# Optimization experiments

Measured on AMD Instinct MI355X. Metric: run time of the kernel, lower is better.

Reference implementation:

```python
import jax, jax.numpy as jnp
import numpy as np

N = 50000          # num nodes
E = 800000         # edges per adjacency (avg degree 16)
NFEAT = 512
NHID = 256
NCLS = 100
LN_EPS = 1e-5


def spmm(rows, cols, vals, feat):
    # sparse [N,N] @ dense [N,F] via gather + segment-sum scatter
    return jax.ops.segment_sum(vals[:, None] * feat[cols], rows, num_segments=N)


def layernorm(h, g, b):
    mu = jnp.mean(h, axis=-1, keepdims=True)
    var = jnp.var(h, axis=-1, keepdims=True)
    return (h - mu) * jax.lax.rsqrt(var + LN_EPS) * g + b


def setup_inputs() -> dict:
    key = jax.random.key(0)
    ks = jax.random.split(key, 20)
    inp = {
        "x": jax.random.normal(ks[0], (N, NFEAT), dtype=jnp.float32),
        "adj_rows": jax.random.randint(ks[1], (4, E), 0, N, dtype=jnp.int32),
        "adj_cols": jax.random.randint(ks[2], (4, E), 0, N, dtype=jnp.int32),
        "adj_vals": jax.random.uniform(ks[3], (4, E), dtype=jnp.float32) / 16.0,
    }
    def lin(k, fin, fout):
        s = 1.0 / np.sqrt(fin)
        kw, kb = jax.random.split(k)
        return (jax.random.uniform(kw, (fin, fout), minval=-s, maxval=s, dtype=jnp.float32),
                jax.random.uniform(kb, (fout,), minval=-s, maxval=s, dtype=jnp.float32))
    # layer 0: GraphSage(nfeat -> nhid), LayerNorm over 2*nhid
    inp["W0"], inp["b0"] = lin(ks[4], NFEAT, NHID)
    inp["ln0_g"] = jnp.ones((2 * NHID,), jnp.float32)
    inp["ln0_b"] = jnp.zeros((2 * NHID,), jnp.float32)
    # layer 1: GCN(2*nhid -> nhid)
    inp["W1"], inp["b1"] = lin(ks[5], 2 * NHID, NHID)
    # layer 2: GraphSage(nhid -> nhid), LayerNorm over 2*nhid
    inp["W2"], inp["b2"] = lin(ks[6], NHID, NHID)
    inp["ln2_g"] = jnp.ones((2 * NHID,), jnp.float32)
    inp["ln2_b"] = jnp.zeros((2 * NHID,), jnp.float32)
    # layer 3: GCN(2*nhid -> nhid)
    inp["W3"], inp["b3"] = lin(ks[7], 2 * NHID, NHID)
    # output linear (nhid -> num_classes)
    inp["Wout"], inp["bout"] = lin(ks[8], NHID, NCLS)
    return inp


def reference(x, adj_rows, adj_cols, adj_vals,
              W0, b0, ln0_g, ln0_b, W1, b1, W2, b2, ln2_g, ln2_b, W3, b3,
              Wout, bout):
    # layer 0: GraphSage — feat = Linear(x); h = LN(concat([feat, A@feat])); ReLU; dropout(p=0)=id
    feat = x @ W0 + b0
    agg = spmm(adj_rows[0], adj_cols[0], adj_vals[0], feat)
    h = jax.nn.relu(layernorm(jnp.concatenate([feat, agg], axis=1), ln0_g, ln0_b))
    # layer 1: GCN — h = A @ Linear(h); ReLU
    h = jax.nn.relu(spmm(adj_rows[1], adj_cols[1], adj_vals[1], h @ W1 + b1))
    # layer 2: GraphSage
    feat = h @ W2 + b2
    agg = spmm(adj_rows[2], adj_cols[2], adj_vals[2], feat)
    h = jax.nn.relu(layernorm(jnp.concatenate([feat, agg], axis=1), ln2_g, ln2_b))
    # layer 3: GCN
    h = jax.nn.relu(spmm(adj_rows[3], adj_cols[3], adj_vals[3], h @ W3 + b3))
    # output head
    return h @ Wout + bout
```

## Files before the change

kernel.cpp:

```cpp
#include <hip/hip_runtime.h>

#define N_NODES 50000
#define E_EDGES 800000
#define NFEAT   512
#define NHID    256
#define NCLS    100
#define LN_EPS  1e-5f

#define NB     196
#define CHUNKA 6144
#define CAPB   6656

typedef __attribute__((ext_vector_type(8))) short bf16x8;
typedef __attribute__((ext_vector_type(4))) float f32x4;

__device__ __forceinline__ ushort bf16_rne(float x) {
    unsigned u = __float_as_uint(x);
    unsigned r = u + 0x7FFFu + ((u >> 16) & 1u);
    return (ushort)(r >> 16);
}
__device__ __forceinline__ float bf16_to_f(ushort h) {
    return __uint_as_float(((unsigned)h) << 16);
}

__device__ __forceinline__ void gload16(const void* g, void* l) {
    __builtin_amdgcn_global_load_lds(
        (const __attribute__((address_space(1))) unsigned int*)g,
        (__attribute__((address_space(3))) unsigned int*)l, 16, 0, 0);
}

__global__ __launch_bounds__(256)
void wsplit_kernel(const float* __restrict__ W, ushort* __restrict__ WT,
                   int K, int Nc, int NP)
{
    const int idx = blockIdx.x * 256 + threadIdx.x;
    if (idx >= NP * K) return;
    const int n = idx / K, k = idx - n * K;
    const float w = (n < Nc) ? W[(size_t)k * Nc + n] : 0.f;
    WT[idx] = bf16_rne(w);
}

__global__ __launch_bounds__(256)
void xconv_kernel(const float* __restrict__ x, ushort* __restrict__ xb, int n8)
{
    const int idx = blockIdx.x * 256 + threadIdx.x;
    if (idx >= n8) return;
    const float4 v0 = ((const float4*)x)[idx * 2];
    const float4 v1 = ((const float4*)x)[idx * 2 + 1];
    bf16x8 h;
    h[0] = (short)bf16_rne(v0.x); h[1] = (short)bf16_rne(v0.y);
    h[2] = (short)bf16_rne(v0.z); h[3] = (short)bf16_rne(v0.w);
    h[4] = (short)bf16_rne(v1.x); h[5] = (short)bf16_rne(v1.y);
    h[6] = (short)bf16_rne(v1.z); h[7] = (short)bf16_rne(v1.w);
    *(bf16x8*)&xb[idx * 8] = h;
}

template<int WF32, int WBF>
__global__ __launch_bounds__(512)
void gemm_mfma_bf16(const ushort* __restrict__ A1, const ushort* __restrict__ A2,
                    int K1, int K, const ushort* __restrict__ BT,
                    const float* __restrict__ bias, float* __restrict__ C,
                    ushort* __restrict__ Cbf, int M, int Nc)
{
    __shared__ __align__(16) ushort Ah[2][128 * 32];
    __shared__ __align__(16) ushort Bh[2][128 * 32];

    const int tid = threadIdx.x;
    const int bm  = blockIdx.x * 128;
    const int bn  = blockIdx.y * 128;
    const int w   = tid >> 6;
    const int l   = tid & 63;
    const int wm  = (w >> 2) * 64;
    const int wn  = (w & 3) * 32;
    const int fr  = l & 15;
    const int fq  = l >> 4;

    const int gro = l >> 2;
    const int gch = ((l & 3) ^ (gro & 3)) * 8;
    const int ldsbase = (16 * w) * 32;

    f32x4 acc[4][2];
    #pragma unroll
    for (int i = 0; i < 4; ++i) {
        acc[i][0] = (f32x4){0.f, 0.f, 0.f, 0.f};
        acc[i][1] = (f32x4){0.f, 0.f, 0.f, 0.f};
    }

    const int K2 = K - K1;
    const int NS = K / 32;

    auto stage = [&](int s, int b) {
        const int k0 = s * 32;
        gload16(&BT[(size_t)(bn + 16 * w + gro) * K + k0 + gch], &Bh[b][ldsbase]);
        const ushort* asrc;
        if (k0 < K1) asrc = &A1[(size_t)(bm + 16 * w + gro) * K1 + k0 + gch];
        else         asrc = &A2[(size_t)(bm + 16 * w + gro) * K2 + (k0 - K1) + gch];
        gload16(asrc, &Ah[b][ldsbase]);
    };

    stage(0, 0);
    __syncthreads();

    int cur = 0;
    for (int s = 0; s < NS; ++s) {
        if (s + 1 < NS) stage(s + 1, cur ^ 1);

        bf16x8 bf[2];
        #pragma unroll
        for (int nf = 0; nf < 2; ++nf) {
            const int r = wn + nf * 16 + fr;
            bf[nf] = *(const bf16x8*)&Bh[cur][r * 32 + ((fq ^ (r & 3)) * 8)];
        }
        #pragma unroll
        for (int mf = 0; mf < 4; ++mf) {
            const int r = wm + mf * 16 + fr;
            const bf16x8 af = *(const bf16x8*)&Ah[cur][r * 32 + ((fq ^ (r & 3)) * 8)];
            acc[mf][0] = __builtin_amdgcn_mfma_f32_16x16x32_bf16(af, bf[0], acc[mf][0], 0, 0, 0);
            acc[mf][1] = __builtin_amdgcn_mfma_f32_16x16x32_bf16(af, bf[1], acc[mf][1], 0, 0, 0);
        }
        __syncthreads();
        cur ^= 1;
    }

    #pragma unroll
    for (int mf = 0; mf < 4; ++mf) {
        #pragma unroll
        for (int r = 0; r < 4; ++r) {
            const int row = bm + wm + mf * 16 + fq * 4 + r;
            if (row >= M) continue;
            #pragma unroll
            for (int nf = 0; nf < 2; ++nf) {
                const int col = bn + wn + nf * 16 + fr;
                if (col < Nc) {
                    const float v = acc[mf][nf][r] + bias[col];
                    if (WF32) C[(size_t)row * Nc + col] = v;
                    if (WBF)  Cbf[(size_t)row * Nc + col] = bf16_rne(v);
                }
            }
        }
    }
}

__global__ __launch_bounds__(256)
void bin_kernel(const int* __restrict__ rows, const int* __restrict__ cols,
                const float* __restrict__ vals, int* __restrict__ bcur,
                int2* __restrict__ est)
{
    __shared__ int cnt[NB];
    __shared__ int scn[256];
    __shared__ int cstart[NB];
    __shared__ int ccur[NB];
    __shared__ int garr[NB];
    __shared__ __align__(16) int2 buf[CHUNKA];

    const int a  = blockIdx.y;
    const int e0 = blockIdx.x * CHUNKA;
    const int n  = min(CHUNKA, E_EDGES - e0);
    const int t  = threadIdx.x;
    const int*   rp = rows + (size_t)a * E_EDGES + e0;
    const int*   cp = cols + (size_t)a * E_EDGES + e0;
    const float* vp = vals + (size_t)a * E_EDGES + e0;

    if (t < NB) cnt[t] = 0;
    __syncthreads();
    for (int i = t; i < n; i += 256) atomicAdd(&cnt[((unsigned)rp[i]) >> 8], 1);
    __syncthreads();

    scn[t] = (t < NB) ? cnt[t] : 0;
    __syncthreads();
    for (int off = 1; off < 256; off <<= 1) {
        const int v = (t >= off) ? scn[t - off] : 0;
        __syncthreads();
        scn[t] += v;
        __syncthreads();
    }
    if (t < NB) {
        const int ex = scn[t] - cnt[t];
        cstart[t] = ex;
        ccur[t]   = ex;
        garr[t]   = atomicAdd(&bcur[a * NB + t], cnt[t]);
    }
    __syncthreads();

    for (int i = t; i < n; i += 256) {
        const unsigned r = (unsigned)rp[i];
        const int b = r >> 8;
        const int p = atomicAdd(&ccur[b], 1);
        buf[p] = make_int2((int)((r << 16) | (unsigned)cp[i]), __float_as_int(vp[i]));
    }
    __syncthreads();

    for (int i = t; i < n; i += 256) {
        const int2 en = buf[i];
        const int b = ((unsigned)en.x) >> 24;
        const int slot = garr[b] + (i - cstart[b]);
        if (slot < CAPB)
            est[((size_t)(a * NB + b)) * CAPB + slot] = en;
    }
}

__global__ __launch_bounds__(256)
void bscan_kernel(const int* __restrict__ bcur, int* __restrict__ bbase)
{
    __shared__ int s[256];
    const int a = blockIdx.x;
    const int t = threadIdx.x;
    const int v = (t < NB) ? bcur[a * NB + t] : 0;
    s[t] = v;
    __syncthreads();
    for (int off = 1; off < 256; off <<= 1) {
        const int u = (t >= off) ? s[t - off] : 0;
        __syncthreads();
        s[t] += u;
        __syncthreads();
    }
    if (t < NB) bbase[a * NB + t] = s[t] - v;
}

__global__ __launch_bounds__(256)
void sort_kernel(const int* __restrict__ bcur, const int* __restrict__ bbase,
                 const int2* __restrict__ est, int2* __restrict__ cpk,
                 int* __restrict__ rowstart)
{
    __shared__ __align__(16) int2 sbuf[CAPB];
    __shared__ __align__(16) int2 obuf[CAPB];
    __shared__ int cnt[256];
    __shared__ int scn[256];
    __shared__ int cur[256];

    const int a = blockIdx.y;
    const int b = blockIdx.x;
    const int t = threadIdx.x;
    const int nb = min(bcur[a * NB + b], CAPB);
    const size_t slots = ((size_t)(a * NB + b)) * CAPB;

    for (int i = t; i < nb; i += 256) sbuf[i] = est[slots + i];
    cnt[t] = 0;
    __syncthreads();
    for (int i = t; i < nb; i += 256)
        atomicAdd(&cnt[(((unsigned)sbuf[i].x) >> 16) & 255], 1);
    __syncthreads();

    scn[t] = cnt[t];
    __syncthreads();
    for (int off = 1; off < 256; off <<= 1) {
        const int v = (t >= off) ? scn[t - off] : 0;
        __syncthreads();
        scn[t] += v;
        __syncthreads();
    }
    const int excl = scn[t] - cnt[t];
    cur[t] = excl;

    const int bb = bbase[a * NB + b];
    const int r0 = b << 8;
    if (r0 + t < N_NODES)
        rowstart[(size_t)a * (N_NODES + 1) + r0 + t] = bb + excl;
    if (b == NB - 1 && t == 0)
        rowstart[(size_t)a * (N_NODES + 1) + N_NODES] = E_EDGES;
    __syncthreads();

    for (int i = t; i < nb; i += 256) {
        const int2 en = sbuf[i];
        const int r = (((unsigned)en.x) >> 16) & 255;
        const int p = atomicAdd(&cur[r], 1);
        obuf[p] = make_int2(en.x & 0xFFFF, en.y);
    }
    __syncthreads();

    int2* co = cpk + (size_t)a * E_EDGES + bb;
    for (int i = t; i < nb; i += 256) co[i] = obuf[i];
}

template<int LNFUSE>
__global__ __launch_bounds__(256)
void spmm_kernel(const int* __restrict__ rowstart, const int2* __restrict__ cpk,
                 const ushort* __restrict__ feat, ushort* __restrict__ out0,
                 ushort* __restrict__ out1, const float* __restrict__ g,
                 const float* __restrict__ be)
{
    const int row  = __builtin_amdgcn_readfirstlane((blockIdx.x * 256 + threadIdx.x) >> 6);
    const int lane = threadIdx.x & 63;

    const int s = __builtin_amdgcn_readfirstlane(rowstart[row]);
    const int e = __builtin_amdgcn_readfirstlane(rowstart[row + 1]);

    const ushort* fbase = feat + lane * 4;
    float ax = 0.f, ay = 0.f, az = 0.f, aw = 0.f;

    for (int j = s; j < e; j += 16) {
        #pragma unroll
        for (int q = 0; q < 16; ++q) {
            if (j + q < e) {
                const int2 ev = cpk[j + q];
                const float v = __int_as_float(ev.y);
                const uint2 f = *(const uint2*)(fbase + (size_t)ev.x * NHID);
                ax += v * __uint_as_float(f.x << 16);
                ay += v * __uint_as_float(f.x & 0xFFFF0000u);
                az += v * __uint_as_float(f.y << 16);
                aw += v * __uint_as_float(f.y & 0xFFFF0000u);
            }
        }
    }

    if (LNFUSE) {
        const uint2 fx = *(const uint2*)(fbase + (size_t)row * NHID);
        float xf[4] = {__uint_as_float(fx.x << 16), __uint_as_float(fx.x & 0xFFFF0000u),
                       __uint_as_float(fx.y << 16), __uint_as_float(fx.y & 0xFFFF0000u)};

        float sum = xf[0] + xf[1] + xf[2] + xf[3] + ax + ay + az + aw;
        #pragma unroll
        for (int m = 1; m < 64; m <<= 1) sum += __shfl_xor(sum, m, 64);
        const float mean = sum * (1.f / 512.f);

        float sq = 0.f;
        #pragma unroll
        for (int jj = 0; jj < 4; ++jj) { const float d = xf[jj] - mean; sq += d * d; }
        { float d; d = ax - mean; sq += d * d; d = ay - mean; sq += d * d;
          d = az - mean; sq += d * d; d = aw - mean; sq += d * d; }
        #pragma unroll
        for (int m = 1; m < 64; m <<= 1) sq += __shfl_xor(sq, m, 64);
        const float rstd = rsqrtf(sq * (1.f / 512.f) + LN_EPS);

        const int col = lane * 4;
        const float av[4] = {ax, ay, az, aw};
        ushort4 o0, o1;
        float t0[4], t1[4];
        #pragma unroll
        for (int jj = 0; jj < 4; ++jj) {
            t0[jj] = fmaxf((xf[jj] - mean) * rstd * g[col + jj] + be[col + jj], 0.f);
            t1[jj] = fmaxf((av[jj] - mean) * rstd * g[256 + col + jj] + be[256 + col + jj], 0.f);
        }
        o0.x = bf16_rne(t0[0]); o0.y = bf16_rne(t0[1]); o0.z = bf16_rne(t0[2]); o0.w = bf16_rne(t0[3]);
        o1.x = bf16_rne(t1[0]); o1.y = bf16_rne(t1[1]); o1.z = bf16_rne(t1[2]); o1.w = bf16_rne(t1[3]);
        *(ushort4*)&out0[(size_t)row * NHID + col] = o0;
        *(ushort4*)&out1[(size_t)row * NHID + col] = o1;
    } else {
        ushort4 o;
        o.x = bf16_rne(fmaxf(ax, 0.f)); o.y = bf16_rne(fmaxf(ay, 0.f));
        o.z = bf16_rne(fmaxf(az, 0.f)); o.w = bf16_rne(fmaxf(aw, 0.f));
        *(ushort4*)&out0[(size_t)row * NHID + lane * 4] = o;
    }
}

extern "C" void kernel_launch(void* const* d_in, const int* in_sizes, int n_in,
                              void* d_out, int out_size, void* d_ws, size_t ws_size,
                              hipStream_t stream)
{
    const float* x    = (const float*)d_in[0];
    const int*   rows = (const int*)  d_in[1];
    const int*   cols = (const int*)  d_in[2];
    const float* vals = (const float*)d_in[3];
    const float* W0   = (const float*)d_in[4];
    const float* b0   = (const float*)d_in[5];
    const float* g0   = (const float*)d_in[6];
    const float* be0  = (const float*)d_in[7];
    const float* W1   = (const float*)d_in[8];
    const float* b1   = (const float*)d_in[9];
    const float* W2   = (const float*)d_in[10];
    const float* b2   = (const float*)d_in[11];
    const float* g2   = (const float*)d_in[12];
    const float* be2  = (const float*)d_in[13];
    const float* W3   = (const float*)d_in[14];
    const float* b3   = (const float*)d_in[15];
    const float* Wout = (const float*)d_in[16];
    const float* bout = (const float*)d_in[17];
    float* out = (float*)d_out;

    char* wsb = (char*)d_ws;
    size_t off = 0;
    auto carve = [&](size_t bytes) { void* p = wsb + off; off += (bytes + 255) & ~(size_t)255; return p; };
    int*    rowstart = (int*)   carve((size_t)4 * (N_NODES + 1) * 4);
    int*    bcur     = (int*)   carve((size_t)4 * NB * 4);
    int*    bbase    = (int*)   carve((size_t)4 * NB * 4);
    int2*   cpk      = (int2*)  carve((size_t)4 * E_EDGES * 8);
    int2*   est      = (int2*)  carve((size_t)4 * NB * CAPB * 8);
    ushort* Xb       = (ushort*)carve((size_t)N_NODES * NFEAT * 2);
    ushort* F        = (ushort*)carve((size_t)N_NODES * NHID * 2);
    ushort* P        = (ushort*)carve((size_t)N_NODES * NHID * 2);
    ushort* Q        = (ushort*)carve((size_t)N_NODES * NHID * 2);
    ushort* G        = (ushort*)carve((size_t)N_NODES * NHID * 2);
    ushort* H        = (ushort*)carve((size_t)N_NODES * NHID * 2);
    ushort* W0T = (ushort*)carve((size_t)256 * 512 * 2);
    ushort* W1T = (ushort*)carve((size_t)256 * 512 * 2);
    ushort* W2T = (ushort*)carve((size_t)256 * 256 * 2);
    ushort* W3T = (ushort*)carve((size_t)256 * 512 * 2);
    ushort* WoT = (ushort*)carve((size_t)128 * 256 * 2);
    carve(131072);

    const dim3 blk(256);
    const dim3 blkg(512);
    const dim3 g_gemm(391, 2);
    const dim3 g_head(391, 1);
    const dim3 g_bin((E_EDGES + CHUNKA - 1) / CHUNKA, 4);
    const dim3 g_sort(NB, 4);
    const int  row_blocks = (N_NODES * 64 + 255) / 256;

    wsplit_kernel<<<(256*512 + 255)/256, blk, 0, stream>>>(W0,   W0T, 512, 256, 256);
    wsplit_kernel<<<(256*512 + 255)/256, blk, 0, stream>>>(W1,   W1T, 512, 256, 256);
    wsplit_kernel<<<(256*256 + 255)/256, blk, 0, stream>>>(W2,   W2T, 256, 256, 256);
    wsplit_kernel<<<(256*512 + 255)/256, blk, 0, stream>>>(W3,   W3T, 512, 256, 256);
    wsplit_kernel<<<(128*256 + 255)/256, blk, 0, stream>>>(Wout, WoT, 256, 100, 128);
    xconv_kernel<<<(N_NODES * NFEAT / 8 + 255)/256, blk, 0, stream>>>(x, Xb, N_NODES * NFEAT / 8);

    hipMemsetAsync(bcur, 0, (size_t)4 * NB * 4, stream);
    bin_kernel<<<g_bin, blk, 0, stream>>>(rows, cols, vals, bcur, est);
    bscan_kernel<<<4, blk, 0, stream>>>(bcur, bbase);
    sort_kernel<<<g_sort, blk, 0, stream>>>(bcur, bbase, est, cpk, rowstart);

    const int* rs0 = rowstart;
    const int* rs1 = rowstart + (N_NODES + 1);
    const int* rs2 = rowstart + 2 * (N_NODES + 1);
    const int* rs3 = rowstart + 3 * (N_NODES + 1);
    const int2* c0 = cpk;
    const int2* c1 = cpk + E_EDGES;
    const int2* c2 = cpk + 2 * (size_t)E_EDGES;
    const int2* c3 = cpk + 3 * (size_t)E_EDGES;

    gemm_mfma_bf16<0,1><<<g_gemm, blkg, 0, stream>>>(Xb, Xb, 512, 512, W0T, b0, nullptr, F, N_NODES, 256);
    spmm_kernel<1><<<row_blocks, blk, 0, stream>>>(rs0, c0, F, P, Q, g0, be0);

    gemm_mfma_bf16<0,1><<<g_gemm, blkg, 0, stream>>>(P, Q, 256, 512, W1T, b1, nullptr, G, N_NODES, 256);
    spmm_kernel<0><<<row_blocks, blk, 0, stream>>>(rs1, c1, G, H, nullptr, nullptr, nullptr);

    gemm_mfma_bf16<0,1><<<g_gemm, blkg, 0, stream>>>(H, H, 256, 256, W2T, b2, nullptr, F, N_NODES, 256);
    spmm_kernel<1><<<row_blocks, blk, 0, stream>>>(rs2, c2, F, P, Q, g2, be2);

    gemm_mfma_bf16<0,1><<<g_gemm, blkg, 0, stream>>>(P, Q, 256, 512, W3T, b3, nullptr, G, N_NODES, 256);
    spmm_kernel<0><<<row_blocks, blk, 0, stream>>>(rs3, c3, G, H, nullptr, nullptr, nullptr);

    gemm_mfma_bf16<1,0><<<g_head, blkg, 0, stream>>>(H, H, 256, 256, WoT, bout, out, nullptr, N_NODES, 100);
}
```

Before: 529.1 us.

## Use 4-wave GEMM tiles, merge weight conversions, and drop LDS staging in sort

The GEMM moves from 8 waves with 64x32 warp tiles to 4 waves with 64x64 warp tiles. Each wave now issues two loads per stage and 16 MFMAs per K step, which raises register use and lowers wave count per block. The five weight-transpose launches become one kernel that dispatches on the flat index. The sort kernel reads bucket entries directly from global memory twice instead of staging them in shared memory, so it uses less LDS and may fit more blocks per CU.

```diff
diff --git a/kernel.cpp b/kernel.cpp
--- a/kernel.cpp
+++ b/kernel.cpp
@@ -30,14 +30,23 @@
 }
 
 __global__ __launch_bounds__(256)
-void wsplit_kernel(const float* __restrict__ W, ushort* __restrict__ WT,
-                   int K, int Nc, int NP)
-{
-    const int idx = blockIdx.x * 256 + threadIdx.x;
-    if (idx >= NP * K) return;
+void wsplit_all(const float* __restrict__ W0, const float* __restrict__ W1,
+                const float* __restrict__ W2, const float* __restrict__ W3,
+                const float* __restrict__ Wo,
+                ushort* __restrict__ W0T, ushort* __restrict__ W1T,
+                ushort* __restrict__ W2T, ushort* __restrict__ W3T,
+                ushort* __restrict__ WoT)
+{
+    int idx = blockIdx.x * 256 + threadIdx.x;
+    const float* W; ushort* WT; int K, Nc;
+    if      (idx < 131072) { W = W0; WT = W0T; K = 512; Nc = 256; }
+    else if (idx < 262144) { idx -= 131072; W = W1; WT = W1T; K = 512; Nc = 256; }
+    else if (idx < 327680) { idx -= 262144; W = W2; WT = W2T; K = 256; Nc = 256; }
+    else if (idx < 458752) { idx -= 327680; W = W3; WT = W3T; K = 512; Nc = 256; }
+    else if (idx < 491520) { idx -= 458752; W = Wo; WT = WoT; K = 256; Nc = 100; }
+    else return;
     const int n = idx / K, k = idx - n * K;
-    const float w = (n < Nc) ? W[(size_t)k * Nc + n] : 0.f;
-    WT[idx] = bf16_rne(w);
+    WT[idx] = bf16_rne((n < Nc) ? W[(size_t)k * Nc + n] : 0.f);
 }
 
 __global__ __launch_bounds__(256)
@@ -56,7 +65,7 @@
 }
 
 template<int WF32, int WBF>
-__global__ __launch_bounds__(512)
+__global__ __launch_bounds__(256)
 void gemm_mfma_bf16(const ushort* __restrict__ A1, const ushort* __restrict__ A2,
                     int K1, int K, const ushort* __restrict__ BT,
                     const float* __restrict__ bias, float* __restrict__ C,
@@ -70,32 +79,38 @@
     const int bn  = blockIdx.y * 128;
     const int w   = tid >> 6;
     const int l   = tid & 63;
-    const int wm  = (w >> 2) * 64;
-    const int wn  = (w & 3) * 32;
+    const int wm  = (w >> 1) * 64;
+    const int wn  = (w & 1) * 64;
     const int fr  = l & 15;
     const int fq  = l >> 4;
 
     const int gro = l >> 2;
     const int gch = ((l & 3) ^ (gro & 3)) * 8;
-    const int ldsbase = (16 * w) * 32;
-
-    f32x4 acc[4][2];
+    const int ldsbase = (32 * w) * 32;
+
+    f32x4 acc[4][4];
     #pragma unroll
-    for (int i = 0; i < 4; ++i) {
-        acc[i][0] = (f32x4){0.f, 0.f, 0.f, 0.f};
-        acc[i][1] = (f32x4){0.f, 0.f, 0.f, 0.f};
-    }
+    for (int i = 0; i < 4; ++i)
+        #pragma unroll
+        for (int j = 0; j < 4; ++j) acc[i][j] = (f32x4){0.f, 0.f, 0.f, 0.f};
 
     const int K2 = K - K1;
     const int NS = K / 32;
 
     auto stage = [&](int s, int b) {
         const int k0 = s * 32;
-        gload16(&BT[(size_t)(bn + 16 * w + gro) * K + k0 + gch], &Bh[b][ldsbase]);
-        const ushort* asrc;
-        if (k0 < K1) asrc = &A1[(size_t)(bm + 16 * w + gro) * K1 + k0 + gch];
-        else         asrc = &A2[(size_t)(bm + 16 * w + gro) * K2 + (k0 - K1) + gch];
-        gload16(asrc, &Ah[b][ldsbase]);
+        gload16(&BT[(size_t)(bn + 32 * w + gro) * K + k0 + gch],      &Bh[b][ldsbase]);
+        gload16(&BT[(size_t)(bn + 32 * w + 16 + gro) * K + k0 + gch], &Bh[b][ldsbase + 512]);
+        const ushort *a0, *a1;
+        if (k0 < K1) {
+            a0 = &A1[(size_t)(bm + 32 * w + gro) * K1 + k0 + gch];
+            a1 = &A1[(size_t)(bm + 32 * w + 16 + gro) * K1 + k0 + gch];
+        } else {
+            a0 = &A2[(size_t)(bm + 32 * w + gro) * K2 + (k0 - K1) + gch];
+            a1 = &A2[(size_t)(bm + 32 * w + 16 + gro) * K2 + (k0 - K1) + gch];
+        }
+        gload16(a0, &Ah[b][ldsbase]);
+        gload16(a1, &Ah[b][ldsbase + 512]);
     };
 
     stage(0, 0);
@@ -105,9 +120,9 @@
     for (int s = 0; s < NS; ++s) {
         if (s + 1 < NS) stage(s + 1, cur ^ 1);
 
-        bf16x8 bf[2];
-        #pragma unroll
-        for (int nf = 0; nf < 2; ++nf) {
+        bf16x8 bf[4];
+        #pragma unroll
+        for (int nf = 0; nf < 4; ++nf) {
             const int r = wn + nf * 16 + fr;
             bf[nf] = *(const bf16x8*)&Bh[cur][r * 32 + ((fq ^ (r & 3)) * 8)];
         }
@@ -115,8 +130,9 @@
         for (int mf = 0; mf < 4; ++mf) {
             const int r = wm + mf * 16 + fr;
             const bf16x8 af = *(const bf16x8*)&Ah[cur][r * 32 + ((fq ^ (r & 3)) * 8)];
-            acc[mf][0] = __builtin_amdgcn_mfma_f32_16x16x32_bf16(af, bf[0], acc[mf][0], 0, 0, 0);
-            acc[mf][1] = __builtin_amdgcn_mfma_f32_16x16x32_bf16(af, bf[1], acc[mf][1], 0, 0, 0);
+            #pragma unroll
+            for (int nf = 0; nf < 4; ++nf)
+                acc[mf][nf] = __builtin_amdgcn_mfma_f32_16x16x32_bf16(af, bf[nf], acc[mf][nf], 0, 0, 0);
         }
         __syncthreads();
         cur ^= 1;
@@ -129,7 +145,7 @@
             const int row = bm + wm + mf * 16 + fq * 4 + r;
             if (row >= M) continue;
             #pragma unroll
-            for (int nf = 0; nf < 2; ++nf) {
+            for (int nf = 0; nf < 4; ++nf) {
                 const int col = bn + wn + nf * 16 + fr;
                 if (col < Nc) {
                     const float v = acc[mf][nf][r] + bias[col];
@@ -222,34 +238,33 @@
                  const int2* __restrict__ est, int2* __restrict__ cpk,
                  int* __restrict__ rowstart)
 {
-    __shared__ __align__(16) int2 sbuf[CAPB];
     __shared__ __align__(16) int2 obuf[CAPB];
     __shared__ int cnt[256];
-    __shared__ int scn[256];
     __shared__ int cur[256];
 
     const int a = blockIdx.y;
     const int b = blockIdx.x;
     const int t = threadIdx.x;
     const int nb = min(bcur[a * NB + b], CAPB);
-    const size_t slots = ((size_t)(a * NB + b)) * CAPB;
-
-    for (int i = t; i < nb; i += 256) sbuf[i] = est[slots + i];
+    const int2* ei = est + ((size_t)(a * NB + b)) * CAPB;
+
     cnt[t] = 0;
     __syncthreads();
     for (int i = t; i < nb; i += 256)
-        atomicAdd(&cnt[(((unsigned)sbuf[i].x) >> 16) & 255], 1);
-    __syncthreads();
-
-    scn[t] = cnt[t];
+        atomicAdd(&cnt[(((unsigned)ei[i].x) >> 16) & 255], 1);
+    __syncthreads();
+
+    int scv = cnt[t];
+    cur[t] = scv;
     __syncthreads();
     for (int off = 1; off < 256; off <<= 1) {
-        const int v = (t >= off) ? scn[t - off] : 0;
-        __syncthreads();
-        scn[t] += v;
-        __syncthreads();
-    }
-    const int excl = scn[t] - cnt[t];
+        const int v = (t >= off) ? cur[t - off] : 0;
+        __syncthreads();
+        cur[t] += v;
+        __syncthreads();
+    }
+    const int excl = cur[t] - scv;
+    __syncthreads();
     cur[t] = excl;
 
     const int bb = bbase[a * NB + b];
@@ -261,7 +276,7 @@
     __syncthreads();
 
     for (int i = t; i < nb; i += 256) {
-        const int2 en = sbuf[i];
+        const int2 en = ei[i];
         const int r = (((unsigned)en.x) >> 16) & 255;
         const int p = atomicAdd(&cur[r], 1);
         obuf[p] = make_int2(en.x & 0xFFFF, en.y);
@@ -389,18 +404,13 @@
     carve(131072);
 
     const dim3 blk(256);
-    const dim3 blkg(512);
     const dim3 g_gemm(391, 2);
     const dim3 g_head(391, 1);
     const dim3 g_bin((E_EDGES + CHUNKA - 1) / CHUNKA, 4);
     const dim3 g_sort(NB, 4);
     const int  row_blocks = (N_NODES * 64 + 255) / 256;
 
-    wsplit_kernel<<<(256*512 + 255)/256, blk, 0, stream>>>(W0,   W0T, 512, 256, 256);
-    wsplit_kernel<<<(256*512 + 255)/256, blk, 0, stream>>>(W1,   W1T, 512, 256, 256);
-    wsplit_kernel<<<(256*256 + 255)/256, blk, 0, stream>>>(W2,   W2T, 256, 256, 256);
-    wsplit_kernel<<<(256*512 + 255)/256, blk, 0, stream>>>(W3,   W3T, 512, 256, 256);
-    wsplit_kernel<<<(128*256 + 255)/256, blk, 0, stream>>>(Wout, WoT, 256, 100, 128);
+    wsplit_all<<<1920, blk, 0, stream>>>(W0, W1, W2, W3, Wout, W0T, W1T, W2T, W3T, WoT);
     xconv_kernel<<<(N_NODES * NFEAT / 8 + 255)/256, blk, 0, stream>>>(x, Xb, N_NODES * NFEAT / 8);
 
     hipMemsetAsync(bcur, 0, (size_t)4 * NB * 4, stream);
@@ -417,17 +427,17 @@
     const int2* c2 = cpk + 2 * (size_t)E_EDGES;
     const int2* c3 = cpk + 3 * (size_t)E_EDGES;
 
-    gemm_mfma_bf16<0,1><<<g_gemm, blkg, 0, stream>>>(Xb, Xb, 512, 512, W0T, b0, nullptr, F, N_NODES, 256);
+    gemm_mfma_bf16<0,1><<<g_gemm, blk, 0, stream>>>(Xb, Xb, 512, 512, W0T, b0, nullptr, F, N_NODES, 256);
     spmm_kernel<1><<<row_blocks, blk, 0, stream>>>(rs0, c0, F, P, Q, g0, be0);
 
-    gemm_mfma_bf16<0,1><<<g_gemm, blkg, 0, stream>>>(P, Q, 256, 512, W1T, b1, nullptr, G, N_NODES, 256);
+    gemm_mfma_bf16<0,1><<<g_gemm, blk, 0, stream>>>(P, Q, 256, 512, W1T, b1, nullptr, G, N_NODES, 256);
     spmm_kernel<0><<<row_blocks, blk, 0, stream>>>(rs1, c1, G, H, nullptr, nullptr, nullptr);
 
-    gemm_mfma_bf16<0,1><<<g_gemm, blkg, 0, stream>>>(H, H, 256, 256, W2T, b2, nullptr, F, N_NODES, 256);
+    gemm_mfma_bf16<0,1><<<g_gemm, blk, 0, stream>>>(H, H, 256, 256, W2T, b2, nullptr, F, N_NODES, 256);
     spmm_kernel<1><<<row_blocks, blk, 0, stream>>>(rs2, c2, F, P, Q, g2, be2);
 
-    gemm_mfma_bf16<0,1><<<g_gemm, blkg, 0, stream>>>(P, Q, 256, 512, W3T, b3, nullptr, G, N_NODES, 256);
+    gemm_mfma_bf16<0,1><<<g_gemm, blk, 0, stream>>>(P, Q, 256, 512, W3T, b3, nullptr, G, N_NODES, 256);
     spmm_kernel<0><<<row_blocks, blk, 0, stream>>>(rs3, c3, G, H, nullptr, nullptr, nullptr);
 
-    gemm_mfma_bf16<1,0><<<g_head, blkg, 0, stream>>>(H, H, 256, 256, WoT, bout, out, nullptr, N_NODES, 100);
-}
+    gemm_mfma_bf16<1,0><<<g_head, blk, 0, stream>>>(H, H, 256, 256, WoT, bout, out, nullptr, N_NODES, 100);
+}
```

Result: slower. 576.9 us (+9.0%).
